# Kernel tuning notes

Measured on AMD Instinct MI355X. Metric: run time of the kernel, lower is better.

The kernel has to match this reference:

```python
import jax, jax.numpy as jnp
import numpy as np

DIST = 200.0
BBOX_SP = 24
N_COARSE = 64
N_BOXES = 10
SAMPLES_ALL = N_COARSE + 2 * N_BOXES  # 84
FR_POS = 10
FR_DIR = 4
NSEM = 50
WID = 256
MERGES = [(39, 41), (27, 26), (28, 26), (29, 26), (30, 26), (31, 26), (9, 8), (35, 13)]


def posenc(x, L):
    f = 2.0 ** jnp.arange(L, dtype=x.dtype)
    xb = x[..., None, :] * f[:, None]                      # [..., L, 3]
    enc = jnp.concatenate([jnp.sin(xb), jnp.cos(xb)], -1)  # [..., L, 6]
    return jnp.concatenate([x, enc.reshape(x.shape[:-1] + (-1,))], -1)


def sample_pdf(bins, weights, n):
    # deterministic inverse-CDF sampling (det=True), bins [B,N,M], weights [B,N,M-1]
    pdf = weights / jnp.sum(weights, -1, keepdims=True)
    cdf = jnp.cumsum(pdf, -1)
    cdf = jnp.concatenate([jnp.zeros_like(cdf[..., :1]), cdf], -1)   # [B,N,M]
    B, N, M = cdf.shape
    u = jnp.linspace(0.0, 1.0, n, dtype=bins.dtype)
    cdf_f = cdf.reshape(B * N, M)
    bins_f = bins.reshape(B * N, M)
    u_f = jnp.broadcast_to(u, (B * N, n))
    inds = jax.vmap(lambda c, uu: jnp.searchsorted(c, uu, side='right'))(cdf_f, u_f)
    below = jnp.clip(inds - 1, 0, M - 1)
    above = jnp.clip(inds, 0, M - 1)
    cdf_b = jnp.take_along_axis(cdf_f, below, 1)
    cdf_a = jnp.take_along_axis(cdf_f, above, 1)
    bin_b = jnp.take_along_axis(bins_f, below, 1)
    bin_a = jnp.take_along_axis(bins_f, above, 1)
    denom = jnp.where(cdf_a - cdf_b < 1e-5, 1.0, cdf_a - cdf_b)
    t = (u_f - cdf_b) / denom
    return (bin_b + t * (bin_a - bin_b)).reshape(B, N, n)


def setup_inputs() -> dict:
    key = jax.random.key(0)
    ks = jax.random.split(key, 16)
    B, N = 1, 2048
    rays_o = jax.random.normal(ks[0], (B, N, 3)) * 2.0
    rays_d = jax.random.normal(ks[1], (B, N, 3))
    rays = jnp.concatenate([rays_o, rays_d], -1)
    near = jax.random.uniform(ks[2], (B, N, N_BOXES), minval=5.0, maxval=150.0)
    far = near + jax.random.uniform(ks[3], (B, N, N_BOXES), minval=5.0, maxval=60.0)
    inst = jax.random.randint(ks[4], (B, N, N_BOXES), 0, 20).astype(jnp.float32)
    label = jax.random.randint(ks[5], (B, N, N_BOXES), 1, NSEM).astype(jnp.float32)
    intersection = jnp.stack([near, far, inst, label], -1)  # [B,N,10,4]
    bg_noise = jax.random.uniform(ks[6], (B, N, SAMPLES_ALL))

    def lin(k, fi, fo):
        return jax.random.normal(k, (fi, fo)) / np.sqrt(fi)

    d_x = 3 + 6 * FR_POS  # 63
    d_d = 3 + 6 * FR_DIR  # 27
    params = dict(
        w_in=lin(ks[7], d_x, WID), b_in=jnp.zeros((WID,)),
        w_h=jax.random.normal(ks[8], (6, WID, WID)) / np.sqrt(WID), b_h=jnp.zeros((6, WID)),
        w_skip=lin(ks[9], WID + d_x, WID), b_skip=jnp.zeros((WID,)),
        w_sigma=lin(ks[10], WID, 1), b_sigma=jnp.zeros((1,)),
        w_feat=lin(ks[11], WID, WID), b_feat=jnp.zeros((WID,)),
        w_rgb1=lin(ks[12], WID + d_d, 128), b_rgb1=jnp.zeros((128,)),
        w_rgb2=lin(ks[13], 128, 3), b_rgb2=jnp.zeros((3,)),
        w_sem=lin(ks[14], WID, NSEM), b_sem=jnp.zeros((NSEM,)),
    )
    out = {'rays': rays, 'intersection': intersection, 'bg_noise': bg_noise}
    out.update(params)
    return out


def reference(rays, intersection, bg_noise, w_in, b_in, w_h, b_h, w_skip, b_skip,
              w_sigma, b_sigma, w_feat, b_feat, w_rgb1, b_rgb1, w_rgb2, b_rgb2,
              w_sem, b_sem):
    B, N, _ = rays.shape
    rays_o, rays_d = rays[..., :3], rays[..., 3:6]
    scale = jnp.linalg.norm(rays_d, axis=-1)  # [B,N]

    # --- ray sampling inside boxes + uniform-PDF resampling ---
    near, far = intersection[..., 0], intersection[..., 1]  # [B,N,10]
    t = jnp.linspace(0.0, 1.0, BBOX_SP)
    z_box = near[..., None] + (far - near)[..., None] * t       # [B,N,10,24]
    z_bound = jnp.concatenate([z_box[..., 0] - 1e-5, z_box[..., -1] + 1e-5], axis=2)  # [B,N,20]
    zf = jnp.sort(z_box.reshape(B, N, -1), axis=2)              # [B,N,240]
    z = sample_pdf(zf, jnp.ones_like(zf[..., 1:]), N_COARSE)    # [B,N,64]
    z = jnp.concatenate([z, z_bound], axis=2)                   # [B,N,84]
    z = jnp.where(z < 0.0, DIST + 20.0 * bg_noise, z)
    z = jnp.sort(z, axis=2)

    # --- NeRF MLP on sample points ---
    xyz = (rays_o[:, :, None] + rays_d[:, :, None] * z[..., None] / scale[..., None, None]) / DIST
    dirs = rays_d / scale[..., None]
    x_enc = posenc(xyz, FR_POS)                                 # [B,N,S,63]
    h = jax.nn.relu(x_enc @ w_in + b_in)
    for i in range(3):
        h = jax.nn.relu(h @ w_h[i] + b_h[i])
    h = jax.nn.relu(jnp.concatenate([h, x_enc], -1) @ w_skip + b_skip)
    for i in range(3, 6):
        h = jax.nn.relu(h @ w_h[i] + b_h[i])
    sigma = (h @ w_sigma + b_sigma)[..., 0]                     # [B,N,S]
    sem = h @ w_sem + b_sem                                     # [B,N,S,50]
    feat = h @ w_feat + b_feat
    d_enc = posenc(dirs, FR_DIR)                                # [B,N,27]
    d_enc = jnp.broadcast_to(d_enc[:, :, None, :], feat.shape[:-1] + (d_enc.shape[-1],))
    hr = jax.nn.relu(jnp.concatenate([feat, d_enc], -1) @ w_rgb1 + b_rgb1)
    rgb = hr @ w_rgb2 + b_rgb2                                  # [B,N,S,3]

    # --- semantic one-hot scatter + boundary masks (no-grad region) ---
    zs = jax.lax.stop_gradient(z)
    nearb = intersection[:, :, None, :, 0]                      # [B,N,1,10]
    farb = intersection[:, :, None, :, 1]
    inside = (zs[..., None] > nearb) & (zs[..., None] < farb)   # [B,N,S,10]
    d1 = zs[..., None] - farb
    d2 = nearb - zs[..., None]
    mask_bound = jnp.any(((d1 > 0) & (d1 < 1e-3)) | ((d2 > 0) & (d2 < 1e-3)), axis=-1)
    labels = intersection[..., 3].astype(jnp.int32)             # [B,N,10]
    oh_box = jax.nn.one_hot(labels, NSEM)                       # [B,N,10,50]
    one_hot = jnp.max(inside[..., None].astype(jnp.float32) * oh_box[:, :, None, :, :], axis=3)
    s0 = one_hot.sum(-1)
    mask_bbox = (zs < DIST) & (s0 == 0.0)
    mask_bg = (zs > DIST) & (s0 == 0.0)
    one_hot = one_hot.at[..., 0].set(jnp.where(mask_bbox, 1.0, one_hot[..., 0]))
    one_hot = one_hot.at[..., 23].set(jnp.where(mask_bg, 1.0, one_hot[..., 23]))
    for src, dst in MERGES:  # training-mode class merging (box/car/park/gate)
        one_hot = one_hot.at[..., dst].set(jnp.maximum(one_hot[..., dst], one_hot[..., src]))
        one_hot = one_hot.at[..., src].set(0.0)
    one_hot = jax.lax.stop_gradient(one_hot)

    # zero density outside boxes and at box boundaries
    sigma = jnp.where(mask_bbox | mask_bound, 0.0, sigma)

    # --- volumetric compositing (raw2outputs_semantic_joint) ---
    z_true = z / scale[..., None]
    dists = jnp.concatenate([z_true[..., 1:] - z_true[..., :-1],
                             jnp.full_like(z_true[..., :1], 1e10)], -1) * scale[..., None]
    alpha = 1.0 - jnp.exp(-jax.nn.relu(sigma) * dists)
    trans = jnp.cumprod(jnp.concatenate([jnp.ones_like(alpha[..., :1]),
                                         1.0 - alpha + 1e-10], -1)[..., :-1], -1)
    w = alpha * trans                                           # [B,N,S]
    rgb_map = jnp.einsum('bns,bnsc->bnc', w, jax.nn.sigmoid(rgb))
    depth = jnp.sum(w * z_true, -1)
    acc = jnp.sum(w, -1)
    sem_map = jnp.einsum('bns,bnsc->bnc', w, sem)
    return jnp.concatenate([rgb_map, depth[..., None], acc[..., None], sem_map], -1)  # [B,N,55]
```

## Files before the change

### kernel.cpp

```cpp
#include <hip/hip_runtime.h>

typedef _Float16 half8 __attribute__((ext_vector_type(8)));
typedef float f32x4 __attribute__((ext_vector_type(4)));

#define NRAYS 2048
#define SAMP 84
#define NPTS (NRAYS*SAMP)
#define SEMSTR 52

#define WT0_OFF   0
#define WTH_OFF   16384
#define WTS_OFF   409600
#define WTHD_OFF  491520
#define WTR1_OFF  573440
#define WTR2_OFF  610304
#define WT_TOTAL  612352
#define NBIAS     2512

#define OFF_WT    ((size_t)0)
#define OFF_BIAS  ((size_t)1224704)
#define OFF_Z     (OFF_BIAS + (size_t)NBIAS*4)
#define OFF_SCALE (OFF_Z + (size_t)NPTS*4)
#define OFF_SIGMA (OFF_SCALE + (size_t)NRAYS*4)
#define OFF_RGB   (OFF_SIGMA + (size_t)NPTS*4)
#define OFF_SEM   (OFF_RGB + (size_t)NPTS*12)

__global__ __launch_bounds__(256) void prep_kernel(
    const float* __restrict__ w_in,  const float* __restrict__ w_h,
    const float* __restrict__ w_skip,const float* __restrict__ w_sigma,
    const float* __restrict__ w_feat,const float* __restrict__ w_rgb1,
    const float* __restrict__ w_rgb2,const float* __restrict__ w_sem,
    const float* __restrict__ b_in,  const float* __restrict__ b_h,
    const float* __restrict__ b_skip,const float* __restrict__ b_sigma,
    const float* __restrict__ b_feat,const float* __restrict__ b_rgb1,
    const float* __restrict__ b_rgb2,const float* __restrict__ b_sem,
    _Float16* __restrict__ wt, float* __restrict__ bias)
{
  int idx = blockIdx.x*256 + threadIdx.x;
  if (idx < WT_TOTAL) {
    float v; int n, k, l, h, q;
    if (idx < WTH_OFF) {
      int r = idx; int F = r >> 10; int rem = r & 1023; int kt = rem >> 9; q = rem & 511;
      l = q >> 3; h = q & 7;
      n = F*16 + (l&15); k = kt*32 + (l>>4)*8 + h;
      v = (k < 63) ? w_in[k*256 + n] : 0.f;
    } else if (idx < WTS_OFF) {
      int r = idx - WTH_OFF; int i = r >> 16; int r2 = r & 65535;
      int F = r2 >> 12; int kt = (r2 >> 9) & 7; q = r2 & 511;
      l = q >> 3; h = q & 7;
      n = F*16 + (l&15); k = kt*32 + (l>>4)*8 + h;
      v = w_h[(i<<16) + (k<<8) + n];
    } else if (idx < WTHD_OFF) {
      int r = idx - WTS_OFF; int F = r / 5120; int rem = r % 5120; int kt = rem >> 9; q = rem & 511;
      l = q >> 3; h = q & 7;
      n = F*16 + (l&15); k = kt*32 + (l>>4)*8 + h;
      v = (k < 319) ? w_skip[k*256 + n] : 0.f;
    } else if (idx < WTR1_OFF) {
      int r = idx - WTHD_OFF; int F = r >> 12; int kt = (r >> 9) & 7; q = r & 511;
      l = q >> 3; h = q & 7;
      n = F*16 + (l&15); k = kt*32 + (l>>4)*8 + h;
      v = (n < 256) ? w_feat[(k<<8) + n]
        : (n < 306) ? w_sem[k*50 + (n-256)]
        : (n == 306)? w_sigma[k] : 0.f;
    } else if (idx < WTR2_OFF) {
      int r = idx - WTR1_OFF; int F = r / 4608; int rem = r % 4608; int kt = rem >> 9; q = rem & 511;
      l = q >> 3; h = q & 7;
      n = F*16 + (l&15); k = kt*32 + (l>>4)*8 + h;
      v = (k < 283) ? w_rgb1[k*128 + n] : 0.f;
    } else {
      int r = idx - WTR2_OFF; int kt = r >> 9; q = r & 511;
      l = q >> 3; h = q & 7;
      n = (l&15); k = kt*32 + (l>>4)*8 + h;
      v = (n < 3) ? w_rgb2[k*3 + n] : 0.f;
    }
    wt[idx] = (_Float16)v;
  } else if (idx < WT_TOTAL + NBIAS) {
    int j = idx - WT_TOTAL; float v;
    if (j < 2048) {
      int i = j >> 8, c = j & 255;
      v = (i==0) ? b_in[c] : (i<4) ? b_h[(i-1)*256+c]
        : (i==4) ? b_skip[c] : b_h[(i-2)*256+c];
    } else if (j < 2368) {
      int c = j - 2048;
      v = (c<256) ? b_feat[c] : (c<306) ? b_sem[c-256]
        : (c==306) ? b_sigma[0] : 0.f;
    } else if (j < 2496) v = b_rgb1[j-2368];
    else { int c = j-2496; v = (c<3) ? b_rgb2[c] : 0.f; }
    bias[j] = v;
  }
}

__global__ __launch_bounds__(256) void sample_kernel(
    const float* __restrict__ rays, const float* __restrict__ inter,
    const float* __restrict__ noise, float* __restrict__ zbuf,
    float* __restrict__ scaleb)
{
  __shared__ float sv[240], ss[240], z2[84];
  const int ray = blockIdx.x, t = threadIdx.x;
  const float* bx = inter + (size_t)ray*40;
  if (t < 240) {
    int b = t/24, j = t%24;
    float nr = bx[b*4], fr = bx[b*4+1];
    float tj = (j==23) ? 1.f : (float)j * (1.f/23.f);
    sv[t] = nr + (fr-nr)*tj;
  }
  __syncthreads();
  if (t < 240) {
    float v = sv[t]; int r = 0;
    for (int i = 0; i < 240; ++i) { float vi = sv[i]; r += (vi < v) || (vi == v && i < t); }
    ss[r] = v;
  }
  __syncthreads();
  if (t < 64) {
    float z;
    if (t == 63) z = ss[239];
    else { int num = t*239; int k = num/63; float f = (float)(num - k*63)*(1.f/63.f);
           z = ss[k] + f*(ss[k+1]-ss[k]); }
    z2[t] = z;
  } else if (t < 84) {
    int b = t - 64;
    z2[t] = (b < 10) ? (bx[b*4] - 1e-5f) : (bx[(b-10)*4+1] + 1e-5f);
  }
  __syncthreads();
  if (t < 84) { float z = z2[t]; if (z < 0.f) z = 200.f + 20.f*noise[(size_t)ray*84 + t]; z2[t] = z; }
  __syncthreads();
  if (t < 84) {
    float v = z2[t]; int r = 0;
    for (int i = 0; i < 84; ++i) { float vi = z2[i]; r += (vi < v) || (vi == v && i < t); }
    zbuf[(size_t)ray*84 + r] = v;
  }
  if (t == 0) {
    float dx = rays[ray*6+3], dy = rays[ray*6+4], dz = rays[ray*6+5];
    scaleb[ray] = sqrtf(dx*dx + dy*dy + dz*dz);
  }
}

#define LDS_A 0u
#define LDS_B 32768u
#define LDS_X 65536u
#define LDS_TOTAL 73728

__device__ __forceinline__ uint32_t laddr(uint32_t base, int m, int k) {
  return base + (uint32_t)(m*512) + (uint32_t)((((k>>3)^(m&7))<<4) + ((k&7)<<1));
}
__device__ __forceinline__ uint32_t laddrX(int m, int k) {
  return LDS_X + (uint32_t)(m*128) + (uint32_t)(((((k>>3)&7)^(m&7))<<4) + ((k&7)<<1));
}
struct __attribute__((aligned(8))) H4 { _Float16 h[4]; };

__device__ __forceinline__ float xenc_val(int j, float x0, float x1, float x2) {
  if (j >= 63) return 0.f;
  if (j < 3) return j==0?x0:(j==1?x1:x2);
  int q = j-3, lf = q/6, r = q%6, ci = r%3;
  float xc = (ci==0)?x0:((ci==1)?x1:x2);
  float arg = xc * (float)(1<<lf);
  return (r<3) ? sinf(arg) : cosf(arg);
}
__device__ __forceinline__ float denc_val(int c, float u0, float u1, float u2) {
  if (c >= 27) return 0.f;
  if (c < 3) return c==0?u0:(c==1?u1:u2);
  int q = c-3, lf = q/6, r = q%6, ci = r%3;
  float uc = (ci==0)?u0:((ci==1)?u1:u2);
  float arg = uc * (float)(1<<lf);
  return (r<3) ? sinf(arg) : cosf(arg);
}

template<int KT, int NF, int MODE, bool RELU, int XSTART>
__device__ __forceinline__ void gemm(uint8_t* smem, uint32_t inb, uint32_t outb,
    const _Float16* __restrict__ WT, int fbase, const float* __restrict__ biasptr,
    int p0, float* __restrict__ sigmaws, _Float16* __restrict__ semws)
{
  constexpr int MF = 4;
  const int t = threadIdx.x;
  const int l = t & 63, w = t >> 6;
  const int lr = l & 15, lg = l >> 4;
  const int wn = w & 3;
  constexpr int DW   = (KT <= 3) ? KT : ((NF > 4) ? 3 : 4);
  constexpr int LEAD = (KT <= 3) ? KT : DW - 1;
  f32x4 acc[NF][MF];
#pragma unroll
  for (int i = 0; i < NF; ++i)
#pragma unroll
    for (int j = 0; j < MF; ++j) acc[i][j] = (f32x4){0.f,0.f,0.f,0.f};
  const _Float16* wb = WT + (size_t)((fbase + wn*NF)*KT)*512 + (size_t)l*8;
  half8 av[DW][NF];
  half8 bv[2][MF];
  auto baddr = [&](int row, int kt)->uint32_t {
    const int kk = kt*32 + lg*8;
    if (XSTART == 0) return laddrX(row, kk);
    if (XSTART < 100000 && kt*32 >= XSTART) return laddrX(row, kk - XSTART);
    return laddr(inb, row, kk);
  };
#pragma unroll
  for (int d = 0; d < LEAD && d < KT; ++d)
#pragma unroll
    for (int nf = 0; nf < NF; ++nf)
      av[d][nf] = *(const half8*)(wb + (size_t)(nf*KT + d)*512);
#pragma unroll
  for (int mf = 0; mf < MF; ++mf)
    bv[0][mf] = *(const half8*)(smem + baddr(mf*16 + lr, 0));
#pragma unroll
  for (int kt = 0; kt < KT; ++kt) {
    if (kt + 1 < KT) {
#pragma unroll
      for (int mf = 0; mf < MF; ++mf)
        bv[(kt+1)&1][mf] = *(const half8*)(smem + baddr(mf*16 + lr, kt+1));
    }
    if (kt + LEAD < KT) {
#pragma unroll
      for (int nf = 0; nf < NF; ++nf)
        av[(kt+LEAD)%DW][nf] = *(const half8*)(wb + (size_t)(nf*KT + kt + LEAD)*512);
    }
    __builtin_amdgcn_sched_barrier(0);
#pragma unroll
    for (int nf = 0; nf < NF; ++nf)
#pragma unroll
      for (int mf = 0; mf < MF; ++mf)
        acc[nf][mf] = __builtin_amdgcn_mfma_f32_16x16x32_f16(av[kt%DW][nf], bv[kt&1][mf], acc[nf][mf], 0, 0, 0);
    __builtin_amdgcn_sched_barrier(0);
  }
#pragma unroll
  for (int nf = 0; nf < NF; ++nf) {
    const int n0 = (wn*NF + nf)*16;
    const int nb = n0 + lg*4;
    const f32x4 bvv = *(const f32x4*)(biasptr + nb);
    if (MODE == 0 || n0 < 256) {
#pragma unroll
      for (int mf = 0; mf < MF; ++mf) {
        const int m = mf*16 + lr;
        f32x4 v = acc[nf][mf] + bvv;
        H4 hh;
#pragma unroll
        for (int r = 0; r < 4; ++r) { float x = v[r]; if (RELU) x = fmaxf(x, 0.f); hh.h[r] = (_Float16)x; }
        *(H4*)(smem + laddr(outb, m, nb)) = hh;
      }
    } else {
      const int cb = nb - 256;
#pragma unroll
      for (int mf = 0; mf < MF; ++mf) {
        const int m = mf*16 + lr;
        const int pp = p0 + m;
        f32x4 v = acc[nf][mf] + bvv;
        if (cb <= 44) {
          H4 hh;
#pragma unroll
          for (int r = 0; r < 4; ++r) hh.h[r] = (_Float16)v[r];
          *(H4*)(semws + (size_t)pp*SEMSTR + cb) = hh;
        } else if (cb == 48) {
          semws[(size_t)pp*SEMSTR + 48] = (_Float16)v[0];
          semws[(size_t)pp*SEMSTR + 49] = (_Float16)v[1];
          sigmaws[pp] = v[2];
        }
      }
    }
  }
}

__device__ __forceinline__ void gemm_rgb2(uint8_t* smem, uint32_t inb,
    const _Float16* __restrict__ WT, const float* __restrict__ bias,
    int p0, float* __restrict__ rgbws)
{
  const int t = threadIdx.x;
  const int l = t & 63, w = t >> 6;
  const int lr = l & 15, lg = l >> 4;
  const int m0 = w*16;
  f32x4 acc = (f32x4){0.f,0.f,0.f,0.f};
#pragma unroll
  for (int kt = 0; kt < 4; ++kt) {
    const int kk = kt*32 + lg*8;
    half8 a = *(const half8*)(WT + (size_t)kt*512 + (size_t)l*8);
    half8 b = *(const half8*)(smem + laddr(inb, m0 + lr, kk));
    acc = __builtin_amdgcn_mfma_f32_16x16x32_f16(a, b, acc, 0, 0, 0);
  }
  const int pp = p0 + m0 + lr;
#pragma unroll
  for (int r = 0; r < 4; ++r) {
    const int n = lg*4 + r;
    if (n < 3) rgbws[(size_t)pp*3 + n] = (float)acc[r] + bias[n];
  }
}

__global__ __launch_bounds__(256,2) void mlp_kernel(
    const float* __restrict__ rays, const float* __restrict__ zbuf,
    const float* __restrict__ scaleb, const _Float16* __restrict__ wt,
    const float* __restrict__ bias, float* __restrict__ sigmaws,
    float* __restrict__ rgbws, _Float16* __restrict__ semws)
{
  extern __shared__ uint8_t smem[];
  const int p0 = blockIdx.x*64;
  const int t = threadIdx.x;
  const int m = t & 63, g = t >> 6;
  const int p = p0 + m;
  const int ray = p / SAMP;
  const float sc = scaleb[ray];
  const float z  = zbuf[p];
  const float ox = rays[ray*6+0], oy = rays[ray*6+1], oz = rays[ray*6+2];
  const float dx = rays[ray*6+3], dy = rays[ray*6+4], dz = rays[ray*6+5];
  const float x0 = (ox + dx*z/sc)/200.f;
  const float x1 = (oy + dy*z/sc)/200.f;
  const float x2 = (oz + dz*z/sc)/200.f;
  const float u0 = dx/sc, u1 = dy/sc, u2 = dz/sc;
  {
    union { _Float16 hv[8]; half8 v; } u8;
#pragma unroll
    for (int hf = 0; hf < 2; ++hf) {
      const int j0 = g*16 + hf*8;
#pragma unroll
      for (int jj = 0; jj < 8; ++jj) u8.hv[jj] = (_Float16)xenc_val(j0+jj, x0, x1, x2);
      *(half8*)(smem + laddrX(m, j0)) = u8.v;
    }
  }
  __syncthreads();
  gemm<2 ,4,0,true ,0     >(smem, LDS_X, LDS_A, wt+WT0_OFF,         0, bias+0,    p0, sigmaws, semws); __syncthreads();
  gemm<8 ,4,0,true ,100000>(smem, LDS_A, LDS_B, wt+WTH_OFF+0*65536, 0, bias+256,  p0, sigmaws, semws); __syncthreads();
  gemm<8 ,4,0,true ,100000>(smem, LDS_B, LDS_A, wt+WTH_OFF+1*65536, 0, bias+512,  p0, sigmaws, semws); __syncthreads();
  gemm<8 ,4,0,true ,100000>(smem, LDS_A, LDS_B, wt+WTH_OFF+2*65536, 0, bias+768,  p0, sigmaws, semws); __syncthreads();
  gemm<10,4,0,true ,256   >(smem, LDS_B, LDS_A, wt+WTS_OFF,         0, bias+1024, p0, sigmaws, semws); __syncthreads();
  {
    union { _Float16 hv[8]; half8 v; } u8;
    const int c0 = g*8;
#pragma unroll
    for (int cc = 0; cc < 8; ++cc) u8.hv[cc] = (_Float16)denc_val(c0+cc, u0, u1, u2);
    *(half8*)(smem + laddrX(m, c0)) = u8.v;
  }
  gemm<8 ,4,0,true ,100000>(smem, LDS_A, LDS_B, wt+WTH_OFF+3*65536, 0, bias+1280, p0, sigmaws, semws); __syncthreads();
  gemm<8 ,4,0,true ,100000>(smem, LDS_B, LDS_A, wt+WTH_OFF+4*65536, 0, bias+1536, p0, sigmaws, semws); __syncthreads();
  gemm<8 ,4,0,true ,100000>(smem, LDS_A, LDS_B, wt+WTH_OFF+5*65536, 0, bias+1792, p0, sigmaws, semws); __syncthreads();
  gemm<8 ,5,1,false,100000>(smem, LDS_B, LDS_A, wt+WTHD_OFF,        0, bias+2048, p0, sigmaws, semws); __syncthreads();
  gemm<9 ,2,0,true ,256   >(smem, LDS_A, LDS_B, wt+WTR1_OFF,        0, bias+2368, p0, sigmaws, semws); __syncthreads();
  gemm_rgb2(smem, LDS_B, wt+WTR2_OFF, bias+2496, p0, rgbws);
}

__global__ __launch_bounds__(128) void comp_kernel(
    const float* __restrict__ inter, const float* __restrict__ zbuf,
    const float* __restrict__ scaleb, const float* __restrict__ sigmaws,
    const float* __restrict__ rgbws, const _Float16* __restrict__ semws,
    float* __restrict__ out)
{
  __shared__ float zt[84], alpha[84], wgt[84];
  const int ray = blockIdx.x, t = threadIdx.x;
  const float sc = scaleb[ray];
  const float* bx = inter + (size_t)ray*40;
  if (t < 84) zt[t] = zbuf[(size_t)ray*84 + t] / sc;
  __syncthreads();
  if (t < 84) {
    const float z = zbuf[(size_t)ray*84 + t];
    bool inside = false, bound = false;
    for (int b = 0; b < 10; ++b) {
      const float nr = bx[b*4], fr = bx[b*4+1];
      inside = inside || (z > nr && z < fr);
      const float d1 = z - fr, d2 = nr - z;
      bound = bound || (d1 > 0.f && d1 < 1e-3f) || (d2 > 0.f && d2 < 1e-3f);
    }
    float sg = sigmaws[(size_t)ray*84 + t];
    const bool bbox = (z < 200.f) && !inside;
    if (bbox || bound) sg = 0.f;
    sg = fmaxf(sg, 0.f);
    const float dist = (t < 83) ? (zt[t+1] - zt[t])*sc : 1e10f*sc;
    alpha[t] = 1.f - expf(-sg*dist);
  }
  __syncthreads();
  if (t == 0) {
    float T = 1.f;
    for (int s = 0; s < 84; ++s) { wgt[s] = alpha[s]*T; T *= (1.f - alpha[s] + 1e-10f); }
  }
  __syncthreads();
  if (t < 55) {
    float a = 0.f;
    const size_t base = (size_t)ray*84;
    if (t < 50) {
      for (int s = 0; s < 84; ++s) a += wgt[s]*(float)semws[(base+s)*SEMSTR + t];
      out[(size_t)ray*55 + 5 + t] = a;
    } else if (t < 53) {
      const int c = t - 50;
      for (int s = 0; s < 84; ++s) { const float r = rgbws[(base+s)*3 + c]; a += wgt[s]/(1.f + expf(-r)); }
      out[(size_t)ray*55 + c] = a;
    } else if (t == 53) {
      for (int s = 0; s < 84; ++s) a += wgt[s]*zt[s];
      out[(size_t)ray*55 + 3] = a;
    } else {
      for (int s = 0; s < 84; ++s) a += wgt[s];
      out[(size_t)ray*55 + 4] = a;
    }
  }
}

extern "C" void kernel_launch(void* const* d_in, const int* in_sizes, int n_in,
                              void* d_out, int out_size, void* d_ws, size_t ws_size,
                              hipStream_t stream) {
  const float* rays   = (const float*)d_in[0];
  const float* inter  = (const float*)d_in[1];
  const float* noise  = (const float*)d_in[2];
  const float* w_in   = (const float*)d_in[3];
  const float* b_in   = (const float*)d_in[4];
  const float* w_h    = (const float*)d_in[5];
  const float* b_h    = (const float*)d_in[6];
  const float* w_skip = (const float*)d_in[7];
  const float* b_skip = (const float*)d_in[8];
  const float* w_sig  = (const float*)d_in[9];
  const float* b_sig  = (const float*)d_in[10];
  const float* w_feat = (const float*)d_in[11];
  const float* b_feat = (const float*)d_in[12];
  const float* w_rgb1 = (const float*)d_in[13];
  const float* b_rgb1 = (const float*)d_in[14];
  const float* w_rgb2 = (const float*)d_in[15];
  const float* b_rgb2 = (const float*)d_in[16];
  const float* w_sem  = (const float*)d_in[17];
  const float* b_sem  = (const float*)d_in[18];

  uint8_t* ws = (uint8_t*)d_ws;
  _Float16* wt    = (_Float16*)(ws + OFF_WT);
  float* bias     = (float*)(ws + OFF_BIAS);
  float* zbuf     = (float*)(ws + OFF_Z);
  float* scaleb   = (float*)(ws + OFF_SCALE);
  float* sigmaws  = (float*)(ws + OFF_SIGMA);
  float* rgbws    = (float*)(ws + OFF_RGB);
  _Float16* semws = (_Float16*)(ws + OFF_SEM);

  prep_kernel<<<dim3((WT_TOTAL + NBIAS + 255)/256), dim3(256), 0, stream>>>(
      w_in, w_h, w_skip, w_sig, w_feat, w_rgb1, w_rgb2, w_sem,
      b_in, b_h, b_skip, b_sig, b_feat, b_rgb1, b_rgb2, b_sem, wt, bias);
  sample_kernel<<<dim3(NRAYS), dim3(256), 0, stream>>>(rays, inter, noise, zbuf, scaleb);
  mlp_kernel<<<dim3(NPTS/64), dim3(256), LDS_TOTAL, stream>>>(
      rays, zbuf, scaleb, wt, bias, sigmaws, rgbws, semws);
  comp_kernel<<<dim3(NRAYS), dim3(128), 0, stream>>>(
      inter, zbuf, scaleb, sigmaws, rgbws, semws, (float*)d_out);
}
```

Measured before the change: 272.5 us.

## Use 128-point tiles with 8 waves and in-place single LDS activation buffer

The MLP kernel now processes 128 points per block with 512 threads, each of 8 waves covering 32 output features across all 128 rows, so each weight fragment loaded from global memory is reused over twice as many points. Activations live in a single 640-byte-stride LDS buffer with the encoding columns appended, and each layer writes its output in place after an extra barrier, replacing the ping-pong A/B buffers. The sem/sigma head is split into a separate call. This trades extra barriers and higher per-wave register use (8 M-fragments) for halved weight traffic per point.

```diff
diff --git a/kernel.cpp b/kernel.cpp
--- a/kernel.cpp
+++ b/kernel.cpp
@@ -135,16 +135,10 @@
   }
 }
 
-#define LDS_A 0u
-#define LDS_B 32768u
-#define LDS_X 65536u
-#define LDS_TOTAL 73728
-
-__device__ __forceinline__ uint32_t laddr(uint32_t base, int m, int k) {
-  return base + (uint32_t)(m*512) + (uint32_t)((((k>>3)^(m&7))<<4) + ((k&7)<<1));
-}
-__device__ __forceinline__ uint32_t laddrX(int m, int k) {
-  return LDS_X + (uint32_t)(m*128) + (uint32_t)(((((k>>3)&7)^(m&7))<<4) + ((k&7)<<1));
+#define LDS_TOTAL 81920
+
+__device__ __forceinline__ uint32_t laddr(int m, int k) {
+  return (uint32_t)(m*640) + (uint32_t)((((k>>3)^(m&7))<<4) + ((k&7)<<1));
 }
 struct __attribute__((aligned(8))) H4 { _Float16 h[4]; };
 
@@ -165,18 +159,19 @@
   return (r<3) ? sinf(arg) : cosf(arg);
 }
 
-template<int KT, int NF, int MODE, bool RELU, int XSTART>
-__device__ __forceinline__ void gemm(uint8_t* smem, uint32_t inb, uint32_t outb,
-    const _Float16* __restrict__ WT, int fbase, const float* __restrict__ biasptr,
+template<int KT, int NF, int WN8, int MODE, bool RELU, int XOFF, bool INPLACE>
+__device__ __forceinline__ void gemm(uint8_t* smem,
+    const _Float16* __restrict__ WT, int fbase, const float* __restrict__ bias0,
     int p0, float* __restrict__ sigmaws, _Float16* __restrict__ semws)
 {
-  constexpr int MF = 4;
+  constexpr int MF = WN8 ? 8 : 4;
   const int t = threadIdx.x;
   const int l = t & 63, w = t >> 6;
   const int lr = l & 15, lg = l >> 4;
-  const int wn = w & 3;
-  constexpr int DW   = (KT <= 3) ? KT : ((NF > 4) ? 3 : 4);
-  constexpr int LEAD = (KT <= 3) ? KT : DW - 1;
+  const int wn = WN8 ? w : (w & 3);
+  const int m0 = WN8 ? 0 : (w >> 2)*64;
+  constexpr int DW   = (KT <= 3) ? KT : 4;
+  constexpr int LEAD = (KT <= 3) ? KT : 3;
   f32x4 acc[NF][MF];
 #pragma unroll
   for (int i = 0; i < NF; ++i)
@@ -185,11 +180,8 @@
   const _Float16* wb = WT + (size_t)((fbase + wn*NF)*KT)*512 + (size_t)l*8;
   half8 av[DW][NF];
   half8 bv[2][MF];
-  auto baddr = [&](int row, int kt)->uint32_t {
-    const int kk = kt*32 + lg*8;
-    if (XSTART == 0) return laddrX(row, kk);
-    if (XSTART < 100000 && kt*32 >= XSTART) return laddrX(row, kk - XSTART);
-    return laddr(inb, row, kk);
+  auto baddr = [&](int mf, int kt)->uint32_t {
+    return laddr(m0 + mf*16 + lr, XOFF + kt*32 + lg*8);
   };
 #pragma unroll
   for (int d = 0; d < LEAD && d < KT; ++d)
@@ -198,13 +190,13 @@
       av[d][nf] = *(const half8*)(wb + (size_t)(nf*KT + d)*512);
 #pragma unroll
   for (int mf = 0; mf < MF; ++mf)
-    bv[0][mf] = *(const half8*)(smem + baddr(mf*16 + lr, 0));
+    bv[0][mf] = *(const half8*)(smem + baddr(mf, 0));
 #pragma unroll
   for (int kt = 0; kt < KT; ++kt) {
     if (kt + 1 < KT) {
 #pragma unroll
       for (int mf = 0; mf < MF; ++mf)
-        bv[(kt+1)&1][mf] = *(const half8*)(smem + baddr(mf*16 + lr, kt+1));
+        bv[(kt+1)&1][mf] = *(const half8*)(smem + baddr(mf, kt+1));
     }
     if (kt + LEAD < KT) {
 #pragma unroll
@@ -219,26 +211,27 @@
         acc[nf][mf] = __builtin_amdgcn_mfma_f32_16x16x32_f16(av[kt%DW][nf], bv[kt&1][mf], acc[nf][mf], 0, 0, 0);
     __builtin_amdgcn_sched_barrier(0);
   }
+  if (INPLACE) __syncthreads();
 #pragma unroll
   for (int nf = 0; nf < NF; ++nf) {
-    const int n0 = (wn*NF + nf)*16;
+    const int n0 = (fbase + wn*NF + nf)*16;
     const int nb = n0 + lg*4;
-    const f32x4 bvv = *(const f32x4*)(biasptr + nb);
+    const f32x4 bvv = *(const f32x4*)(bias0 + nb);
     if (MODE == 0 || n0 < 256) {
 #pragma unroll
       for (int mf = 0; mf < MF; ++mf) {
-        const int m = mf*16 + lr;
+        const int m = m0 + mf*16 + lr;
         f32x4 v = acc[nf][mf] + bvv;
         H4 hh;
 #pragma unroll
         for (int r = 0; r < 4; ++r) { float x = v[r]; if (RELU) x = fmaxf(x, 0.f); hh.h[r] = (_Float16)x; }
-        *(H4*)(smem + laddr(outb, m, nb)) = hh;
+        *(H4*)(smem + laddr(m, nb)) = hh;
       }
     } else {
       const int cb = nb - 256;
 #pragma unroll
       for (int mf = 0; mf < MF; ++mf) {
-        const int m = mf*16 + lr;
+        const int m = m0 + mf*16 + lr;
         const int pp = p0 + m;
         f32x4 v = acc[nf][mf] + bvv;
         if (cb <= 44) {
@@ -256,7 +249,7 @@
   }
 }
 
-__device__ __forceinline__ void gemm_rgb2(uint8_t* smem, uint32_t inb,
+__device__ __forceinline__ void gemm_rgb2(uint8_t* smem,
     const _Float16* __restrict__ WT, const float* __restrict__ bias,
     int p0, float* __restrict__ rgbws)
 {
@@ -267,9 +260,8 @@
   f32x4 acc = (f32x4){0.f,0.f,0.f,0.f};
 #pragma unroll
   for (int kt = 0; kt < 4; ++kt) {
-    const int kk = kt*32 + lg*8;
     half8 a = *(const half8*)(WT + (size_t)kt*512 + (size_t)l*8);
-    half8 b = *(const half8*)(smem + laddr(inb, m0 + lr, kk));
+    half8 b = *(const half8*)(smem + laddr(m0 + lr, kt*32 + lg*8));
     acc = __builtin_amdgcn_mfma_f32_16x16x32_f16(a, b, acc, 0, 0, 0);
   }
   const int pp = p0 + m0 + lr;
@@ -280,16 +272,16 @@
   }
 }
 
-__global__ __launch_bounds__(256,2) void mlp_kernel(
+__global__ __launch_bounds__(512,2) void mlp_kernel(
     const float* __restrict__ rays, const float* __restrict__ zbuf,
     const float* __restrict__ scaleb, const _Float16* __restrict__ wt,
     const float* __restrict__ bias, float* __restrict__ sigmaws,
     float* __restrict__ rgbws, _Float16* __restrict__ semws)
 {
   extern __shared__ uint8_t smem[];
-  const int p0 = blockIdx.x*64;
+  const int p0 = blockIdx.x*128;
   const int t = threadIdx.x;
-  const int m = t & 63, g = t >> 6;
+  const int m = t & 127, g = t >> 7;
   const int p = p0 + m;
   const int ray = p / SAMP;
   const float sc = scaleb[ray];
@@ -307,28 +299,29 @@
       const int j0 = g*16 + hf*8;
 #pragma unroll
       for (int jj = 0; jj < 8; ++jj) u8.hv[jj] = (_Float16)xenc_val(j0+jj, x0, x1, x2);
-      *(half8*)(smem + laddrX(m, j0)) = u8.v;
-    }
-  }
-  __syncthreads();
-  gemm<2 ,4,0,true ,0     >(smem, LDS_X, LDS_A, wt+WT0_OFF,         0, bias+0,    p0, sigmaws, semws); __syncthreads();
-  gemm<8 ,4,0,true ,100000>(smem, LDS_A, LDS_B, wt+WTH_OFF+0*65536, 0, bias+256,  p0, sigmaws, semws); __syncthreads();
-  gemm<8 ,4,0,true ,100000>(smem, LDS_B, LDS_A, wt+WTH_OFF+1*65536, 0, bias+512,  p0, sigmaws, semws); __syncthreads();
-  gemm<8 ,4,0,true ,100000>(smem, LDS_A, LDS_B, wt+WTH_OFF+2*65536, 0, bias+768,  p0, sigmaws, semws); __syncthreads();
-  gemm<10,4,0,true ,256   >(smem, LDS_B, LDS_A, wt+WTS_OFF,         0, bias+1024, p0, sigmaws, semws); __syncthreads();
+      *(half8*)(smem + laddr(m, 256 + j0)) = u8.v;
+    }
+  }
+  __syncthreads();
+  gemm<2 ,2,1,0,true ,256,false>(smem, wt+WT0_OFF,         0,  bias+0,    p0, sigmaws, semws); __syncthreads();
+  gemm<8 ,2,1,0,true ,0  ,true >(smem, wt+WTH_OFF+0*65536, 0,  bias+256,  p0, sigmaws, semws); __syncthreads();
+  gemm<8 ,2,1,0,true ,0  ,true >(smem, wt+WTH_OFF+1*65536, 0,  bias+512,  p0, sigmaws, semws); __syncthreads();
+  gemm<8 ,2,1,0,true ,0  ,true >(smem, wt+WTH_OFF+2*65536, 0,  bias+768,  p0, sigmaws, semws); __syncthreads();
+  gemm<10,2,1,0,true ,0  ,true >(smem, wt+WTS_OFF,         0,  bias+1024, p0, sigmaws, semws); __syncthreads();
   {
     union { _Float16 hv[8]; half8 v; } u8;
     const int c0 = g*8;
 #pragma unroll
     for (int cc = 0; cc < 8; ++cc) u8.hv[cc] = (_Float16)denc_val(c0+cc, u0, u1, u2);
-    *(half8*)(smem + laddrX(m, c0)) = u8.v;
-  }
-  gemm<8 ,4,0,true ,100000>(smem, LDS_A, LDS_B, wt+WTH_OFF+3*65536, 0, bias+1280, p0, sigmaws, semws); __syncthreads();
-  gemm<8 ,4,0,true ,100000>(smem, LDS_B, LDS_A, wt+WTH_OFF+4*65536, 0, bias+1536, p0, sigmaws, semws); __syncthreads();
-  gemm<8 ,4,0,true ,100000>(smem, LDS_A, LDS_B, wt+WTH_OFF+5*65536, 0, bias+1792, p0, sigmaws, semws); __syncthreads();
-  gemm<8 ,5,1,false,100000>(smem, LDS_B, LDS_A, wt+WTHD_OFF,        0, bias+2048, p0, sigmaws, semws); __syncthreads();
-  gemm<9 ,2,0,true ,256   >(smem, LDS_A, LDS_B, wt+WTR1_OFF,        0, bias+2368, p0, sigmaws, semws); __syncthreads();
-  gemm_rgb2(smem, LDS_B, wt+WTR2_OFF, bias+2496, p0, rgbws);
+    *(half8*)(smem + laddr(m, 256 + c0)) = u8.v;
+  }
+  gemm<8 ,2,1,0,true ,0  ,true >(smem, wt+WTH_OFF+3*65536, 0,  bias+1280, p0, sigmaws, semws); __syncthreads();
+  gemm<8 ,2,1,0,true ,0  ,true >(smem, wt+WTH_OFF+4*65536, 0,  bias+1536, p0, sigmaws, semws); __syncthreads();
+  gemm<8 ,2,1,0,true ,0  ,true >(smem, wt+WTH_OFF+5*65536, 0,  bias+1792, p0, sigmaws, semws); __syncthreads();
+  gemm<8 ,1,0,1,false,0  ,false>(smem, wt+WTHD_OFF,        16, bias+2048, p0, sigmaws, semws);
+  gemm<8 ,2,1,0,false,0  ,true >(smem, wt+WTHD_OFF,        0,  bias+2048, p0, sigmaws, semws); __syncthreads();
+  gemm<9 ,1,1,0,true ,0  ,true >(smem, wt+WTR1_OFF,        0,  bias+2368, p0, sigmaws, semws); __syncthreads();
+  gemm_rgb2(smem, wt+WTR2_OFF, bias+2496, p0, rgbws);
 }
 
 __global__ __launch_bounds__(128) void comp_kernel(
@@ -421,7 +414,7 @@
       w_in, w_h, w_skip, w_sig, w_feat, w_rgb1, w_rgb2, w_sem,
       b_in, b_h, b_skip, b_sig, b_feat, b_rgb1, b_rgb2, b_sem, wt, bias);
   sample_kernel<<<dim3(NRAYS), dim3(256), 0, stream>>>(rays, inter, noise, zbuf, scaleb);
-  mlp_kernel<<<dim3(NPTS/64), dim3(256), LDS_TOTAL, stream>>>(
+  mlp_kernel<<<dim3(NPTS/128), dim3(512), LDS_TOTAL, stream>>>(
       rays, zbuf, scaleb, wt, bias, sigmaws, rgbws, semws);
   comp_kernel<<<dim3(NRAYS), dim3(128), 0, stream>>>(
       inter, zbuf, scaleb, sigmaws, rgbws, semws, (float*)d_out);
```

Result: slower. 286.4 us (+5.1%).
